# Performance work log

Measured on AMD Instinct MI355X. Metric: run time of the kernel, lower is better.

The kernel has to match this reference:

```python
import jax, jax.numpy as jnp
from jax import lax
import numpy as np

B, T, C, L, K, LS = 128, 64, 6625, 25, 6, 25
ALPHA, SMOOTH_TAIL, BLANK = 0.1, 0.01, 0


def setup_inputs() -> dict:
    key = jax.random.key(0)
    k1, k2, k3, k4, k5 = jax.random.split(key, 5)
    preds = jax.random.normal(k1, (B, T, C), jnp.float32)
    text = jax.random.randint(k2, (B, L), 1, C)            # labels avoid blank=0
    length = jax.random.randint(k3, (B,), 10, L + 1)       # master target lengths
    preds_size = jnp.full((B,), T, jnp.int32)              # full time length per sample
    smooth_text = jax.random.randint(k4, (B, K, LS), 1, C)
    smooth_length = jax.random.randint(k5, (B, K), 5, LS + 1)
    return dict(preds=preds, text=text, preds_size=preds_size, length=length,
                smooth_text=smooth_text, smooth_length=smooth_length)


def ctc_nll(log_probs, sample_idx, targets, input_lens, target_lens):
    """Batched CTC negative log likelihood (torch.nn.CTCLoss math, zero_infinity).
    log_probs: [T, Bsrc, C] log-softmax; sample_idx: [N] -> Bsrc (lets N targets
    share logits without materializing [T, N, C]); targets: [N, Lmax]."""
    Tt = log_probs.shape[0]
    N, Lt = targets.shape
    S = 2 * Lt + 1
    NEG = jnp.float32(-1e30)
    ext = jnp.full((N, S), BLANK, dtype=targets.dtype).at[:, 1::2].set(targets)
    ext_m2 = jnp.pad(ext[:, :-2], ((0, 0), (2, 0)), constant_values=BLANK)
    allow_skip = (ext != BLANK) & (ext != ext_m2)          # [N, S]

    def frame(lp_t):                                        # [Bsrc,C] -> [N,S]
        return jnp.take_along_axis(lp_t[sample_idx], ext, axis=1)

    lp0 = frame(log_probs[0])
    alpha = jnp.full((N, S), NEG).at[:, 0].set(lp0[:, 0]).at[:, 1].set(lp0[:, 1])

    def step(alpha, xs):
        t, lp_t = xs
        s1 = jnp.pad(alpha[:, :-1], ((0, 0), (1, 0)), constant_values=NEG)
        s2 = jnp.where(allow_skip,
                       jnp.pad(alpha[:, :-2], ((0, 0), (2, 0)), constant_values=NEG), NEG)
        m = jnp.maximum(alpha, jnp.maximum(s1, s2))
        tot = m + jnp.log(jnp.exp(alpha - m) + jnp.exp(s1 - m) + jnp.exp(s2 - m))
        new = tot + frame(lp_t)
        return jnp.where((t < input_lens)[:, None], new, alpha), None

    alpha, _ = lax.scan(step, alpha, (jnp.arange(1, Tt), log_probs[1:]))
    il = (2 * target_lens)[:, None]                         # final blank position
    a_blank = jnp.take_along_axis(alpha, il, axis=1)[:, 0]
    a_char = jnp.take_along_axis(alpha, jnp.maximum(il - 1, 0), axis=1)[:, 0]
    nll = -jnp.logaddexp(a_blank, a_char)
    return jnp.where(nll > 1e29, 0.0, nll)                  # zero_infinity


def _confidence_beam1(lp):
    """CTC prefix beam search with beam_size=1 on one sample. lp: [T, C] log-probs.
    Returns length-normalized prefix probability as the confidence score."""
    Cc = lp.shape[1]
    NEG = jnp.float32(-1e30)
    cs = jnp.arange(Cc)

    def step(state, lp_t):
        lpb, lpnb, last = state
        tot = jnp.logaddexp(lpb, lpnb)
        new_pb = tot + lp_t[BLANK]
        rep = jnp.where(last >= 0, lpnb + lp_t[jnp.maximum(last, 0)], NEG)
        keep = jnp.logaddexp(new_pb, rep)                   # keep same prefix
        ext = jnp.where(cs == last, lpb, tot) + lp_t        # extend by char c
        ext = ext.at[BLANK].set(NEG)
        best_c = jnp.argmax(ext)
        best_ext = ext[best_c]
        take_ext = best_ext > keep
        return (jnp.where(take_ext, NEG, new_pb),
                jnp.where(take_ext, best_ext, rep),
                jnp.where(take_ext, best_c.astype(jnp.int32), last)), None

    init = (jnp.float32(0.0), NEG, jnp.int32(-1))
    (lpb, lpnb, _), _ = lax.scan(step, init, lp)
    score = jnp.logaddexp(lpb, lpnb)
    return jnp.exp(score / lp.shape[0])


def reference(preds, text, preds_size, length, smooth_text, smooth_length):
    lp = jax.nn.log_softmax(preds, axis=2)                  # [B, T, C]
    lp_tbc = jnp.transpose(lp, (1, 0, 2))                   # [T, B, C]
    conf = lax.stop_gradient(jax.vmap(_confidence_beam1)(lp))  # no_grad block

    # master CTC loss (reduction='mean': nll / target_len, then batch mean)
    nll_m = ctc_nll(lp_tbc, jnp.arange(B), text, preds_size, length)
    loss_master = jnp.mean(nll_m / length.astype(lp.dtype))

    # smoothing CTC losses: K hypotheses per sample share that sample's logits
    idx_s = jnp.repeat(jnp.arange(B), K)
    nll_s = ctc_nll(lp_tbc, idx_s, smooth_text.reshape(B * K, LS),
                    jnp.full((B * K,), T, jnp.int32), smooth_length.reshape(B * K))
    loss_cal = jnp.mean((nll_s / smooth_length.reshape(-1).astype(lp.dtype)).reshape(B, K), axis=1)

    ranking = SMOOTH_TAIL + (1.0 - SMOOTH_TAIL) * (1.0 - conf) ** 2
    return loss_master + jnp.mean(ALPHA * ranking * loss_cal)
```

## Files before the change

kernel.cpp:

```cpp
#include <hip/hip_runtime.h>
#include <cstddef>

#define BB   128
#define TT   64
#define CC   6625
#define LL   25
#define KK   6
#define LSS  25
#define SS   51
#define NEG  (-1e30f)
#define FNEG (-3.4e38f)
#define PIVOT 16.0f

#define NCTC       (BB + BB * KK)
#define CTC_BLOCKS (NCTC / 4)

__device__ __forceinline__ float lae(float a, float b) {
    float m = fmaxf(a, b);
    float n = fminf(a, b);
    return m + __logf(1.0f + __expf(n - m));
}

__global__ __launch_bounds__(256, 8) void row_stats_k(
    const float* __restrict__ preds,
    float* __restrict__ lse_t, float* __restrict__ t1v, float* __restrict__ t2v,
    int* __restrict__ t1i, int* __restrict__ t2i, float* __restrict__ cal)
{
    if (blockIdx.x == 0 && threadIdx.x < BB) cal[threadIdx.x] = 0.0f;

    int wave = threadIdx.x >> 6, lane = threadIdx.x & 63;
    int r = blockIdx.x * 4 + wave;
    const float* row = preds + (size_t)r * CC;

    float s0 = 0.0f, s1 = 0.0f, s2 = 0.0f, s3 = 0.0f;
    float v1 = FNEG, v2 = FNEG;
    int   i1 = 0x7fffffff, i2 = 0x7fffffff;

    auto top2 = [&](float x, int c) {
        bool g1 = (x > v1);
        bool g2 = (x > v2);
        v2 = g1 ? v1 : (g2 ? x : v2);
        i2 = g1 ? i1 : (g2 ? c : i2);
        v1 = g1 ? x : v1;
        i1 = g1 ? c : i1;
    };
    auto proc4 = [&](float4 x, int c) {
        s0 += __expf(x.x - PIVOT);
        s1 += __expf(x.y - PIVOT);
        s2 += __expf(x.z - PIVOT);
        s3 += __expf(x.w - PIVOT);
        top2((c == 0) ? FNEG : x.x, c);
        top2(x.y, c + 1);
        top2(x.z, c + 2);
        top2(x.w, c + 3);
    };

    int h = (4 - (r & 3)) & 3;
    if (lane < h) {
        float x = row[lane];
        s0 += __expf(x - PIVOT);
        if (lane > 0) top2(x, lane);
    }

    const float4* vp = (const float4*)(row + h);
    int nv = (CC - h) >> 2;

    #pragma unroll
    for (int g = 0; g < 5; ++g) {
        float4 xr[5];
        #pragma unroll
        for (int k = 0; k < 5; ++k) xr[k] = vp[(g * 5 + k) * 64 + lane];
        #pragma unroll
        for (int k = 0; k < 5; ++k) {
            int idx = (g * 5 + k) * 64 + lane;
            proc4(xr[k], h + idx * 4);
        }
    }
    {
        int idx = 1600 + lane;
        if (idx < nv) proc4(vp[idx], h + idx * 4);
    }
    {
        int t0 = h + nv * 4;
        if (lane < CC - t0) {
            float x = row[t0 + lane];
            s0 += __expf(x - PIVOT);
            top2(x, t0 + lane);
        }
    }

    float s = (s0 + s1) + (s2 + s3);
    for (int off = 32; off > 0; off >>= 1) {
        s += __shfl_xor(s, off);
        float w1 = __shfl_xor(v1, off); int j1 = __shfl_xor(i1, off);
        float w2 = __shfl_xor(v2, off); int j2 = __shfl_xor(i2, off);
        bool b1 = (w1 > v1) || (w1 == v1 && j1 < i1);
        bool b2a = (v1 > w2) || (v1 == w2 && i1 < j2);
        bool b2b = (w1 > v2) || (w1 == v2 && j1 < i2);
        float nv2 = b1 ? (b2a ? v1 : w2) : (b2b ? w1 : v2);
        int   ni2 = b1 ? (b2a ? i1 : j2) : (b2b ? j1 : i2);
        v1 = b1 ? w1 : v1; i1 = b1 ? j1 : i1;
        v2 = nv2; i2 = ni2;
    }

    if (lane == 0) {
        int b = r >> 6, t = r & 63;
        int tr = t * BB + b;
        lse_t[tr] = PIVOT + __logf(s);
        t1v[tr] = v1; t1i[tr] = i1;
        t2v[tr] = v2; t2i[tr] = i2;
    }
}

__global__ __launch_bounds__(256) void ctc_beam_k(
    const float* __restrict__ preds, const float* __restrict__ lse_t,
    const float* __restrict__ t1v, const float* __restrict__ t2v,
    const int* __restrict__ t1i, const int* __restrict__ t2i,
    const int* __restrict__ text, const int* __restrict__ length,
    const int* __restrict__ preds_size,
    const int* __restrict__ smooth_text, const int* __restrict__ smooth_length,
    float* __restrict__ nllm, float* __restrict__ cal, float* __restrict__ ranking)
{
    if (blockIdx.x == CTC_BLOCKS) {
        int b = threadIdx.x;
        if (b >= BB) return;
        const float* pb = preds + (size_t)b * TT * CC;
        float lpb = 0.0f, lpnb = NEG;
        int last = -1;
        float pf0[8];
        #pragma unroll
        for (int i = 0; i < 8; ++i) pf0[i] = pb[(size_t)i * CC];
        float lplast_raw = 0.0f;
        for (int t = 0; t < TT; ++t) {
            int tr = t * BB + b;
            float lse = lse_t[tr];
            float w1 = t1v[tr]; int j1 = t1i[tr];
            float w2 = t2v[tr]; int j2 = t2i[tr];
            float lp0 = pf0[t & 7] - lse;
            if (t + 8 < TT) pf0[t & 7] = pb[(size_t)(t + 8) * CC];
            float lplast = (last >= 0) ? (lplast_raw - lse) : NEG;
            float tot = lae(lpb, lpnb);
            float new_pb = tot + lp0;
            float rep = (last >= 0) ? (lpnb + lplast) : NEG;
            float keep = lae(new_pb, rep);
            float best_ext; int best_c;
            if (j1 == last) {
                float eA = lpb + (w1 - lse);
                float eB = tot + (w2 - lse);
                if (eA > eB || (eA == eB && last < j2)) { best_ext = eA; best_c = last; }
                else                                    { best_ext = eB; best_c = j2; }
            } else {
                best_ext = tot + (w1 - lse);
                best_c = j1;
            }
            bool take = best_ext > keep;
            lpb  = take ? NEG : new_pb;
            lpnb = take ? best_ext : rep;
            last = take ? best_c : last;
            if (t + 1 < TT && last >= 0) lplast_raw = pb[(size_t)(t + 1) * CC + last];
        }
        float score = lae(lpb, lpnb);
        float conf = __expf(score * (1.0f / TT));
        float om = 1.0f - conf;
        ranking[b] = 0.01f + 0.99f * om * om;
        return;
    }

    int wave = threadIdx.x >> 6, lane = threadIdx.x & 63;
    int n = blockIdx.x * 4 + wave;
    if (n >= NCTC) return;
    bool master = n < BB;
    int b, tlen, input_len;
    const int* tgt;
    if (master) {
        b = n; tgt = text + (size_t)n * LL; tlen = length[n]; input_len = preds_size[b];
    } else {
        int ns = n - BB;
        b = ns / KK; tgt = smooth_text + (size_t)ns * LSS; tlen = smooth_length[ns]; input_len = TT;
    }

    int s = lane;
    int ext = 0; bool skipok = false;
    if (s < SS && (s & 1)) {
        int li = (s - 1) >> 1;
        ext = tgt[li];
        skipok = (ext != 0) && (li == 0 || ext != tgt[li - 1]);
    }

    const float* pb = preds + (size_t)b * TT * CC;
    float lse_l = lse_t[lane * BB + b];

    float lse0 = __shfl(lse_l, 0);
    float alpha = NEG;
    if (s < 2) alpha = pb[ext] - lse0;

    float pf[8];
    #pragma unroll
    for (int i = 0; i < 8; ++i) pf[i] = pb[(size_t)(1 + i) * CC + ext];
    for (int t = 1; t < TT; ++t) {
        int slot = (t - 1) & 7;
        float lp = pf[slot] - __shfl(lse_l, t);
        if (t + 8 < TT) pf[slot] = pb[(size_t)(t + 8) * CC + ext];
        float a0 = alpha;
        float a1 = __shfl_up(alpha, 1); a1 = (lane >= 1) ? a1 : NEG;
        float a2 = __shfl_up(alpha, 2); a2 = (lane >= 2 && skipok) ? a2 : NEG;
        float m = fmaxf(a0, fmaxf(a1, a2));
        float tot = m + __logf(__expf(a0 - m) + __expf(a1 - m) + __expf(a2 - m));
        float anew = tot + lp;
        alpha = (t < input_len) ? anew : alpha;
    }

    int il = 2 * tlen;
    float a_bl = __shfl(alpha, il);
    float a_ch = __shfl(alpha, il > 0 ? il - 1 : 0);
    float nll = -lae(a_bl, a_ch);
    if (nll > 1e29f) nll = 0.0f;
    if (lane == 0) {
        float v = nll / (float)tlen;
        if (master) nllm[b] = v;
        else        atomicAdd(&cal[b], v * (1.0f / KK));
    }
}

__global__ __launch_bounds__(128) void final_k(
    const float* __restrict__ nllm, const float* __restrict__ ranking,
    const float* __restrict__ cal, float* __restrict__ out)
{
    int b = threadIdx.x;
    float v = nllm[b] + 0.1f * ranking[b] * cal[b];
    for (int off = 32; off > 0; off >>= 1) v += __shfl_xor(v, off);
    __shared__ float sv[2];
    if ((b & 63) == 0) sv[b >> 6] = v;
    __syncthreads();
    if (b == 0) out[0] = (sv[0] + sv[1]) * (1.0f / BB);
}

extern "C" void kernel_launch(void* const* d_in, const int* in_sizes, int n_in,
                              void* d_out, int out_size, void* d_ws, size_t ws_size,
                              hipStream_t stream)
{
    const float* preds         = (const float*)d_in[0];
    const int*   text          = (const int*)d_in[1];
    const int*   preds_size    = (const int*)d_in[2];
    const int*   length        = (const int*)d_in[3];
    const int*   smooth_text   = (const int*)d_in[4];
    const int*   smooth_length = (const int*)d_in[5];
    float* out = (float*)d_out;

    const int RT = BB * TT;
    float* ws     = (float*)d_ws;
    float* lse_t  = ws;
    float* t1v    = ws + RT;
    float* t2v    = ws + 2 * RT;
    int*   t1i    = (int*)(ws + 3 * RT);
    int*   t2i    = (int*)(ws + 4 * RT);
    float* ranking = ws + 5 * RT;
    float* nllm    = ranking + BB;
    float* cal     = nllm + BB;

    row_stats_k<<<RT / 4, 256, 0, stream>>>(preds, lse_t, t1v, t2v, t1i, t2i, cal);
    ctc_beam_k<<<CTC_BLOCKS + 1, 256, 0, stream>>>(preds, lse_t, t1v, t2v, t1i, t2i,
                                                   text, length, preds_size,
                                                   smooth_text, smooth_length,
                                                   nllm, cal, ranking);
    final_k<<<1, 128, 0, stream>>>(nllm, ranking, cal, out);
}
```

Before: 353.3 us.

## Factor log-sum-exp out of CTC/beam recurrences; software-pipeline row-stats loads

Every path in the alignment lattice picks exactly one symbol per frame, so the per-frame log-normaliser is a common additive offset. The CTC and beam recurrences therefore run on raw logits and subtract the summed LSE once at the end, which removes a per-step shuffle and subtraction from the serial loop. The row-stats kernel also switches to a rolling 6-deep prefetch buffer and issues the head, tail and remainder loads up front. The risk is float precision: the unnormalised alpha values grow larger in magnitude, and the beam argmax comparisons are made on raw values.

Measured after the change: 394.4 us. 1.12x slower.

```diff
diff --git a/kernel.cpp b/kernel.cpp
--- a/kernel.cpp
+++ b/kernel.cpp
@@ -31,6 +31,17 @@
     int wave = threadIdx.x >> 6, lane = threadIdx.x & 63;
     int r = blockIdx.x * 4 + wave;
     const float* row = preds + (size_t)r * CC;
+
+    int h = (4 - (r & 3)) & 3;
+    const float4* vp = (const float4*)(row + h);
+    int nv = (CC - h) >> 2;
+    int t0 = h + (nv << 2);
+
+    float headx = (lane < h) ? row[lane] : FNEG;
+    float tailx = (lane < CC - t0) ? row[t0 + lane] : FNEG;
+    int   remidx = 1600 + lane;
+    bool  remv = remidx < nv;
+    float4 remx = vp[remv ? remidx : 0];
 
     float s0 = 0.0f, s1 = 0.0f, s2 = 0.0f, s3 = 0.0f;
     float v1 = FNEG, v2 = FNEG;
@@ -55,38 +66,24 @@
         top2(x.w, c + 3);
     };
 
-    int h = (4 - (r & 3)) & 3;
+    float4 buf[6];
+    #pragma unroll
+    for (int k = 0; k < 6; ++k) buf[k] = vp[k * 64 + lane];
+    #pragma unroll
+    for (int k = 0; k < 25; ++k) {
+        float4 x = buf[k % 6];
+        if (k + 6 < 25) buf[k % 6] = vp[(k + 6) * 64 + lane];
+        proc4(x, h + (k * 64 + lane) * 4);
+    }
+
     if (lane < h) {
-        float x = row[lane];
-        s0 += __expf(x - PIVOT);
-        if (lane > 0) top2(x, lane);
-    }
-
-    const float4* vp = (const float4*)(row + h);
-    int nv = (CC - h) >> 2;
-
-    #pragma unroll
-    for (int g = 0; g < 5; ++g) {
-        float4 xr[5];
-        #pragma unroll
-        for (int k = 0; k < 5; ++k) xr[k] = vp[(g * 5 + k) * 64 + lane];
-        #pragma unroll
-        for (int k = 0; k < 5; ++k) {
-            int idx = (g * 5 + k) * 64 + lane;
-            proc4(xr[k], h + idx * 4);
-        }
-    }
-    {
-        int idx = 1600 + lane;
-        if (idx < nv) proc4(vp[idx], h + idx * 4);
-    }
-    {
-        int t0 = h + nv * 4;
-        if (lane < CC - t0) {
-            float x = row[t0 + lane];
-            s0 += __expf(x - PIVOT);
-            top2(x, t0 + lane);
-        }
+        s0 += __expf(headx - PIVOT);
+        if (lane > 0) top2(headx, lane);
+    }
+    if (remv) proc4(remx, h + (remidx << 2));
+    if (lane < CC - t0) {
+        s0 += __expf(tailx - PIVOT);
+        top2(tailx, t0 + lane);
     }
 
     float s = (s0 + s1) + (s2 + s3);
@@ -125,6 +122,11 @@
         int b = threadIdx.x;
         if (b >= BB) return;
         const float* pb = preds + (size_t)b * TT * CC;
+
+        float sum_lse = 0.0f;
+        #pragma unroll 8
+        for (int t = 0; t < TT; ++t) sum_lse += lse_t[t * BB + b];
+
         float lpb = 0.0f, lpnb = NEG;
         int last = -1;
         float pf0[8];
@@ -133,24 +135,22 @@
         float lplast_raw = 0.0f;
         for (int t = 0; t < TT; ++t) {
             int tr = t * BB + b;
-            float lse = lse_t[tr];
             float w1 = t1v[tr]; int j1 = t1i[tr];
             float w2 = t2v[tr]; int j2 = t2i[tr];
-            float lp0 = pf0[t & 7] - lse;
+            float lp0 = pf0[t & 7];
             if (t + 8 < TT) pf0[t & 7] = pb[(size_t)(t + 8) * CC];
-            float lplast = (last >= 0) ? (lplast_raw - lse) : NEG;
             float tot = lae(lpb, lpnb);
             float new_pb = tot + lp0;
-            float rep = (last >= 0) ? (lpnb + lplast) : NEG;
+            float rep = (last >= 0) ? (lpnb + lplast_raw) : NEG;
             float keep = lae(new_pb, rep);
             float best_ext; int best_c;
             if (j1 == last) {
-                float eA = lpb + (w1 - lse);
-                float eB = tot + (w2 - lse);
+                float eA = lpb + w1;
+                float eB = tot + w2;
                 if (eA > eB || (eA == eB && last < j2)) { best_ext = eA; best_c = last; }
                 else                                    { best_ext = eB; best_c = j2; }
             } else {
-                best_ext = tot + (w1 - lse);
+                best_ext = tot + w1;
                 best_c = j1;
             }
             bool take = best_ext > keep;
@@ -159,7 +159,7 @@
             last = take ? best_c : last;
             if (t + 1 < TT && last >= 0) lplast_raw = pb[(size_t)(t + 1) * CC + last];
         }
-        float score = lae(lpb, lpnb);
+        float score = lae(lpb, lpnb) - sum_lse;
         float conf = __expf(score * (1.0f / TT));
         float om = 1.0f - conf;
         ranking[b] = 0.01f + 0.99f * om * om;
@@ -188,18 +188,19 @@
     }
 
     const float* pb = preds + (size_t)b * TT * CC;
-    float lse_l = lse_t[lane * BB + b];
-
-    float lse0 = __shfl(lse_l, 0);
+
+    float sum_lse = (lane < input_len) ? lse_t[lane * BB + b] : 0.0f;
+    for (int off = 32; off > 0; off >>= 1) sum_lse += __shfl_xor(sum_lse, off);
+
     float alpha = NEG;
-    if (s < 2) alpha = pb[ext] - lse0;
+    if (s < 2) alpha = pb[ext];
 
     float pf[8];
     #pragma unroll
     for (int i = 0; i < 8; ++i) pf[i] = pb[(size_t)(1 + i) * CC + ext];
     for (int t = 1; t < TT; ++t) {
         int slot = (t - 1) & 7;
-        float lp = pf[slot] - __shfl(lse_l, t);
+        float lp = pf[slot];
         if (t + 8 < TT) pf[slot] = pb[(size_t)(t + 8) * CC + ext];
         float a0 = alpha;
         float a1 = __shfl_up(alpha, 1); a1 = (lane >= 1) ? a1 : NEG;
@@ -213,7 +214,7 @@
     int il = 2 * tlen;
     float a_bl = __shfl(alpha, il);
     float a_ch = __shfl(alpha, il > 0 ? il - 1 : 0);
-    float nll = -lae(a_bl, a_ch);
+    float nll = sum_lse - lae(a_bl, a_ch);
     if (nll > 1e29f) nll = 0.0f;
     if (lane == 0) {
         float v = nll / (float)tlen;
```
